# Performance work log

Measured on AMD Instinct MI355X. Metric: run time of the kernel, lower is better.

The kernel has to match this reference:

```python
import jax, jax.numpy as jnp
import numpy as np

N = 16384          # batch of signals
DIM_T = 256        # time steps per signal
DT = 0.01          # integration dt (intg_lev=1 -> dt_intg = dt)
NUF = 256          # num_units_feat
HID_XI = 128       # hidlayers_xi
HID_AUX = 64       # hidlayers_aux1_dec
LEN_INTG = DIM_T   # (dim_t-1)*intg_lev + 1 with intg_lev=1


def _linear_init(key, fan_in, fan_out):
    # torch nn.Linear default: U(-1/sqrt(fan_in), 1/sqrt(fan_in))
    s = 1.0 / np.sqrt(fan_in)
    kw, kb = jax.random.split(key)
    W = jax.random.uniform(kw, (fan_in, fan_out), minval=-s, maxval=s, dtype=jnp.float32)
    b = jax.random.uniform(kb, (fan_out,), minval=-s, maxval=s, dtype=jnp.float32)
    return W, b


def setup_inputs() -> dict:
    key = jax.random.key(0)
    ks = jax.random.split(key, 12)
    data = jax.random.normal(ks[0], (N, DIM_T), dtype=jnp.float32)
    omega = jax.random.normal(ks[1], (N, 1), dtype=jnp.float32)
    eps = jax.random.normal(ks[2], (N, 1), dtype=jnp.float32)
    # feature extractor (mlp branch): [dim_t+1 -> 256 -> 256], relu after both (actfun_output=True)
    W_feat1, b_feat1 = _linear_init(ks[3], DIM_T + 1, NUF)
    W_feat2, b_feat2 = _linear_init(ks[4], NUF, NUF)
    # xi mean head: MLP [256 -> 128 -> 1] then Softplus
    W_xim1, b_xim1 = _linear_init(ks[5], NUF, HID_XI)
    W_xim2, b_xim2 = _linear_init(ks[6], HID_XI, 1)
    # xi lnvar head: MLP [256 -> 128 -> 1]
    W_xil1, b_xil1 = _linear_init(ks[7], NUF, HID_XI)
    W_xil2, b_xil2 = _linear_init(ks[8], HID_XI, 1)
    # decoder aux1 MLP: [dim_z_aux1+1=2 -> 64 -> 1]
    W_aux1, b_aux1 = _linear_init(ks[9], 2, HID_AUX)
    W_aux2, b_aux2 = _linear_init(ks[10], HID_AUX, 1)
    return dict(data=data, omega=omega, eps=eps,
                W_feat1=W_feat1, b_feat1=b_feat1, W_feat2=W_feat2, b_feat2=b_feat2,
                W_xim1=W_xim1, b_xim1=b_xim1, W_xim2=W_xim2, b_xim2=b_xim2,
                W_xil1=W_xil1, b_xil1=b_xil1, W_xil2=W_xil2, b_xil2=b_xil2,
                W_aux1=W_aux1, b_aux1=b_aux1, W_aux2=W_aux2, b_aux2=b_aux2)


def reference(data, omega, eps,
              W_feat1, b_feat1, W_feat2, b_feat2,
              W_xim1, b_xim1, W_xim2, b_xim2,
              W_xil1, b_xil1, W_xil2, b_xil2,
              W_aux1, b_aux1, W_aux2, b_aux2):
    relu = jax.nn.relu
    # ---- encode_xi ----
    x_ = jnp.concatenate([data, omega], axis=1)                 # [n, dim_t+1]
    feat = relu(relu(x_ @ W_feat1 + b_feat1) @ W_feat2 + b_feat2)  # [n, 256]
    xi_mean = jax.nn.softplus(relu(feat @ W_xim1 + b_xim1) @ W_xim2 + b_xim2)  # [n, 1]
    xi_lnvar = relu(feat @ W_xil1 + b_xil1) @ W_xil2 + b_xil2                  # [n, 1]
    # ---- draw (reparameterization + clamp to feasible range [0, 1]) ----
    xi = xi_mean + jnp.exp(0.5 * xi_lnvar) * eps
    xi = jnp.clip(xi, 0.0, 1.0)
    # ---- decode: Euler odeint over LEN_INTG steps of state yy=[y, dy/dt] ----
    init_y = data[:, :1]                                        # [n, 1]
    initcond = jnp.concatenate([init_y, jnp.zeros_like(init_y)], axis=1)  # [n, 2]

    def step(yy, _):
        # physics: d[y, v]/dt = [v, 0]; aux MLP adds acceleration from (z_aux1=omega, y)
        aux_in = jnp.concatenate([omega, yy[:, :1]], axis=1)    # [n, 2]
        acc = relu(aux_in @ W_aux1 + b_aux1) @ W_aux2 + b_aux2  # [n, 1]
        dyy = jnp.concatenate([yy[:, 1:2], acc], axis=1)        # [n, 2]
        return yy + DT * dyy, yy

    _, yy_seq = jax.lax.scan(step, initcond, None, length=LEN_INTG)  # [len_intg, n, 2]
    y_seq = yy_seq[:, :, 0].T                                   # [n, dim_t] (intg_lev=1)
    t_intg = DT * jnp.arange(LEN_INTG, dtype=jnp.float32)       # [dim_t]
    x_PAB = jnp.exp(-jnp.abs(xi) * t_intg[None, :]) * y_seq     # [n, dim_t]
    return xi_mean, xi_lnvar, x_PAB
```

## Files before the change

kernel.cpp:

```cpp
#include <hip/hip_runtime.h>
#include <math.h>

#define NROWS 16384
#define DT_C 0.01f

typedef short s16x8 __attribute__((ext_vector_type(8)));
typedef float f32x4 __attribute__((ext_vector_type(4)));
typedef float f32x2 __attribute__((ext_vector_type(2)));

__device__ __forceinline__ unsigned short f2bf(float f) {
    unsigned u = __float_as_uint(f);
    u += 0x7fffu + ((u >> 16) & 1u);
    return (unsigned short)(u >> 16);
}
__device__ __forceinline__ unsigned pack2bf(float a, float b) {
    return (unsigned)f2bf(a) | ((unsigned)f2bf(b) << 16);
}
__device__ __forceinline__ float swz1(float v){ return __int_as_float(__builtin_amdgcn_ds_swizzle(__float_as_int(v), 0x041F)); }
__device__ __forceinline__ float swz2(float v){ return __int_as_float(__builtin_amdgcn_ds_swizzle(__float_as_int(v), 0x081F)); }
__device__ __forceinline__ float swz4(float v){ return __int_as_float(__builtin_amdgcn_ds_swizzle(__float_as_int(v), 0x101F)); }

__global__ __launch_bounds__(256) void prep_k(
    const float* __restrict__ Wf1, const float* __restrict__ Wf2,
    const float* __restrict__ Wm1, const float* __restrict__ Wl1,
    const float* __restrict__ bm1, const float* __restrict__ bl1,
    unsigned short* __restrict__ wpack, float* __restrict__ biasH)
{
    const int id = blockIdx.x * 256 + threadIdx.x;
    const int n  = id & 255;
    const int k8 = (id >> 8) & 31;
    const int s  = id >> 13;

    unsigned short tmp[8];
    #pragma unroll
    for (int j = 0; j < 8; ++j) {
        const int k = k8 * 8 + j;
        float v;
        if (s == 0)      v = Wf1[k * 256 + n];
        else if (s == 1) v = Wf2[k * 256 + n];
        else             v = (n < 128) ? Wm1[k * 128 + n] : Wl1[k * 128 + n - 128];
        tmp[j] = f2bf(v);
    }
    *(uint4*)&wpack[((s * 32 + k8) * 256 + n) * 8] = *(const uint4*)tmp;

    if (id < 256) biasH[id] = (id < 128) ? bm1[id] : bl1[id - 128];
}

__global__ __launch_bounds__(256, 2) void fused_k(
    const float* __restrict__ data, const float* __restrict__ omega,
    const float* __restrict__ eps_g,
    const unsigned short* __restrict__ wpack, const float* __restrict__ biasH,
    const float* __restrict__ bf1, const float* __restrict__ bf2,
    const float* __restrict__ w256g,
    const float* __restrict__ Wm2, const float* __restrict__ bm2,
    const float* __restrict__ Wl2, const float* __restrict__ bl2,
    const float* __restrict__ Wa1, const float* __restrict__ ba1,
    const float* __restrict__ Wa2, const float* __restrict__ ba2,
    float* __restrict__ out_mean, float* __restrict__ out_lnvar,
    float* __restrict__ xout)
{
    __shared__ unsigned short As1[8192];
    __shared__ unsigned short Hs[8192];
    __shared__ float headsF[32 * 256];
    __shared__ float omg[32];
    __shared__ float xiS[32];

    const int tid  = threadIdx.x;
    const int wid  = tid >> 6;
    const int lane = tid & 63;
    const int ln   = lane & 15;
    const int quad = lane >> 4;
    const int r0   = blockIdx.x * 32;

    {
        #pragma unroll
        for (int g2 = 0; g2 < 8; ++g2) {
            const int unit = g2 * 256 + tid;
            const int m    = unit >> 6;
            const int c16  = unit & 63;
            const int kblk = c16 >> 1;
            const int h    = c16 & 1;
            const float4 v = *(const float4*)&data[(size_t)(r0 + m) * 256 + c16 * 4];
            unsigned* d = (unsigned*)&As1[((kblk * 32) + (m ^ (kblk & 7))) * 8 + h * 4];
            d[0] = pack2bf(v.x, v.y);
            d[1] = pack2bf(v.z, v.w);
        }
        if (tid < 32) omg[tid] = omega[r0 + tid];
    }

    f32x4 acc[2][4];

    auto seed = [&](const float* bias) {
        #pragma unroll
        for (int nt = 0; nt < 4; ++nt) {
            const float b = bias[wid * 64 + nt * 16 + ln];
            acc[0][nt] = f32x4{b, b, b, b};
            acc[1][nt] = acc[0][nt];
        }
    };

    auto run_stage = [&](const unsigned short* Ap, const unsigned short* wp) {
        #pragma unroll
        for (int c = 0; c < 4; ++c) {
            #pragma unroll
            for (int kk = 0; kk < 2; ++kk) {
                const int kb   = kk * 4 + quad;
                const int kblk = c * 8 + kb;
                const int f    = kblk & 7;
                s16x8 b0 = *(const s16x8*)&wp[((size_t)(kblk * 256) + wid * 64 + 0 * 16 + ln) * 8];
                s16x8 b1 = *(const s16x8*)&wp[((size_t)(kblk * 256) + wid * 64 + 1 * 16 + ln) * 8];
                s16x8 b2 = *(const s16x8*)&wp[((size_t)(kblk * 256) + wid * 64 + 2 * 16 + ln) * 8];
                s16x8 b3 = *(const s16x8*)&wp[((size_t)(kblk * 256) + wid * 64 + 3 * 16 + ln) * 8];
                s16x8 a0 = *(const s16x8*)&Ap[(kblk * 32 + (ln ^ f)) * 8];
                s16x8 a1 = *(const s16x8*)&Ap[(kblk * 32 + ((ln ^ f) + 16)) * 8];
                acc[0][0] = __builtin_amdgcn_mfma_f32_16x16x32_bf16(a0, b0, acc[0][0], 0, 0, 0);
                acc[1][0] = __builtin_amdgcn_mfma_f32_16x16x32_bf16(a1, b0, acc[1][0], 0, 0, 0);
                acc[0][1] = __builtin_amdgcn_mfma_f32_16x16x32_bf16(a0, b1, acc[0][1], 0, 0, 0);
                acc[1][1] = __builtin_amdgcn_mfma_f32_16x16x32_bf16(a1, b1, acc[1][1], 0, 0, 0);
                acc[0][2] = __builtin_amdgcn_mfma_f32_16x16x32_bf16(a0, b2, acc[0][2], 0, 0, 0);
                acc[1][2] = __builtin_amdgcn_mfma_f32_16x16x32_bf16(a1, b2, acc[1][2], 0, 0, 0);
                acc[0][3] = __builtin_amdgcn_mfma_f32_16x16x32_bf16(a0, b3, acc[0][3], 0, 0, 0);
                acc[1][3] = __builtin_amdgcn_mfma_f32_16x16x32_bf16(a1, b3, acc[1][3], 0, 0, 0);
            }
        }
    };

    auto write_packed = [&](unsigned short* dst, bool addOm) {
        #pragma unroll
        for (int nt = 0; nt < 4; ++nt) {
            const int col = wid * 64 + nt * 16 + ln;
            const int kg  = col >> 3, f = kg & 7, jj = col & 7;
            const float wo = addOm ? w256g[col] : 0.f;
            #pragma unroll
            for (int mt = 0; mt < 2; ++mt) {
                #pragma unroll
                for (int r = 0; r < 4; ++r) {
                    const int row = mt * 16 + quad * 4 + r;
                    float v = acc[mt][nt][r];
                    if (addOm) v = fmaf(omg[row], wo, v);
                    v = fmaxf(v, 0.f);
                    dst[(kg * 32 + (row ^ f)) * 8 + jj] = f2bf(v);
                }
            }
        }
    };

    __syncthreads();
    seed(bf1);
    run_stage(As1, wpack);
    write_packed(Hs, true);
    __syncthreads();
    seed(bf2);
    run_stage(Hs, wpack + 65536);
    write_packed(As1, false);
    __syncthreads();
    seed(biasH);
    run_stage(As1, wpack + 131072);
    #pragma unroll
    for (int nt = 0; nt < 4; ++nt) {
        const int col = wid * 64 + nt * 16 + ln;
        #pragma unroll
        for (int mt = 0; mt < 2; ++mt) {
            #pragma unroll
            for (int r = 0; r < 4; ++r) {
                const int row = mt * 16 + quad * 4 + r;
                headsF[row * 256 + ((col + row * 8) & 255)] = fmaxf(acc[mt][nt][r], 0.f);
            }
        }
    }
    __syncthreads();

    {
        const int m = tid >> 3, l = tid & 7;
        float pm = 0.f, pl = 0.f;
        #pragma unroll
        for (int q = 0; q < 4; ++q) {
            const int c0 = l * 16 + q * 4;
            const float4 hm = *(const float4*)&headsF[m * 256 + ((c0 + m * 8) & 255)];
            const float4 wm = *(const float4*)&Wm2[c0];
            const float4 hl = *(const float4*)&headsF[m * 256 + ((128 + c0 + m * 8) & 255)];
            const float4 wl = *(const float4*)&Wl2[c0];
            pm = fmaf(hm.w, wm.w, fmaf(hm.z, wm.z, fmaf(hm.y, wm.y, fmaf(hm.x, wm.x, pm))));
            pl = fmaf(hl.w, wl.w, fmaf(hl.z, wl.z, fmaf(hl.y, wl.y, fmaf(hl.x, wl.x, pl))));
        }
        pm += swz1(pm); pm += swz2(pm); pm += swz4(pm);
        pl += swz1(pl); pl += swz2(pl); pl += swz4(pl);
        if (l == 0) {
            const float xm  = pm + bm2[0];
            const float mean = fmaxf(xm, 0.f) + log1pf(expf(-fabsf(xm)));
            const float lnv  = pl + bl2[0];
            out_mean[r0 + m]  = mean;
            out_lnvar[r0 + m] = lnv;
            float xi = mean + expf(0.5f * lnv) * eps_g[r0 + m];
            xiS[m] = fminf(fmaxf(xi, 0.f), 1.f);
        }
    }
    __syncthreads();

    {
        const int r   = tid >> 3;
        const int l   = tid & 7;
        const int row = r0 + r;
        const float om = omg[r];
        const float xi = xiS[r];
        const float s  = expf(-xi * DT_C);
        const float pseed = ba2[0] * 0.125f;

        f32x2 w1v[4], Av[4], w2v[4];
        #pragma unroll
        for (int i = 0; i < 4; ++i) {
            const f32x2 w0 = *(const f32x2*)&Wa1[l * 8 + i * 2];
            const f32x2 bb = *(const f32x2*)&ba1[l * 8 + i * 2];
            w1v[i] = *(const f32x2*)&Wa1[64 + l * 8 + i * 2];
            w2v[i] = *(const f32x2*)&Wa2[l * 8 + i * 2];
            Av[i]  = f32x2{fmaf(om, w0.x, bb.x), fmaf(om, w0.y, bb.y)};
        }

        auto partial = [&](float y) -> float {
            const f32x2 y2 = f32x2{y, y};
            f32x2 acc2 = f32x2{pseed, 0.f};
            #pragma unroll
            for (int i = 0; i < 4; ++i) {
                f32x2 h = __builtin_elementwise_fma(y2, w1v[i], Av[i]);
                h = __builtin_elementwise_max(h, f32x2{0.f, 0.f});
                acc2 = __builtin_elementwise_fma(h, w2v[i], acc2);
            }
            return acc2.x + acc2.y;
        };

        const float y0 = data[(size_t)row * 256];
        float ym = y0;
        float yc = y0;
        const float DT2 = DT_C * DT_C;

        float p = partial(ym);
        p += swz1(p); p += swz2(p); p += swz4(p);
        float pr = p;

        float d = 1.f;
        float* orow = xout + (size_t)row * 256 + l * 4;

        for (int tb = 0; tb < 8; ++tb) {
            float cur[4];
            #pragma unroll
            for (int j = 0; j < 32; ++j) {
                const float m_ = d * ym;
                if ((j >> 2) == l) cur[j & 3] = m_;
                d *= s;
                float pn = partial(yc);
                pn += swz1(pn); pn += swz2(pn); pn += swz4(pn);
                const float ynext = fmaf(DT2, pr, fmaf(2.f, yc, -ym));
                ym = yc; yc = ynext; pr = pn;
            }
            *(float4*)&orow[tb * 32] = *(const float4*)cur;
        }
    }
}

extern "C" void kernel_launch(void* const* d_in, const int* in_sizes, int n_in,
                              void* d_out, int out_size, void* d_ws, size_t ws_size,
                              hipStream_t stream)
{
    const float* data    = (const float*)d_in[0];
    const float* omega   = (const float*)d_in[1];
    const float* eps     = (const float*)d_in[2];
    const float* W_feat1 = (const float*)d_in[3];
    const float* b_feat1 = (const float*)d_in[4];
    const float* W_feat2 = (const float*)d_in[5];
    const float* b_feat2 = (const float*)d_in[6];
    const float* W_xim1  = (const float*)d_in[7];
    const float* b_xim1  = (const float*)d_in[8];
    const float* W_xim2  = (const float*)d_in[9];
    const float* b_xim2  = (const float*)d_in[10];
    const float* W_xil1  = (const float*)d_in[11];
    const float* b_xil1  = (const float*)d_in[12];
    const float* W_xil2  = (const float*)d_in[13];
    const float* b_xil2  = (const float*)d_in[14];
    const float* W_aux1  = (const float*)d_in[15];
    const float* b_aux1  = (const float*)d_in[16];
    const float* W_aux2  = (const float*)d_in[17];
    const float* b_aux2  = (const float*)d_in[18];

    float* out_mean  = (float*)d_out;
    float* out_lnvar = out_mean + NROWS;
    float* out_x     = out_lnvar + NROWS;

    unsigned short* wpack = (unsigned short*)d_ws;
    float* biasH = (float*)((char*)d_ws + 3 * 32 * 256 * 8 * 2);

    prep_k<<<96, 256, 0, stream>>>(W_feat1, W_feat2, W_xim1, W_xil1,
                                   b_xim1, b_xil1, wpack, biasH);
    fused_k<<<512, 256, 0, stream>>>(data, omega, eps, wpack, biasH,
                                     b_feat1, b_feat2, W_feat1 + 256 * 256,
                                     W_xim2, b_xim2, W_xil2, b_xil2,
                                     W_aux1, b_aux1, W_aux2, b_aux2,
                                     out_mean, out_lnvar, out_x);
}
```

Before: 145.7 us.

## Run ODE integration before MLP encoder and apply decay as a post-pass

The Euler recurrence for y no longer depends on xi, so it now runs first, right after the data tile is loaded, and writes the raw y trajectory to the output. The exp(-xi·t) decay is applied afterwards by reading back and rescaling the output row. Cross-lane reductions switch from ds_swizzle to DPP row operations, and shared memory is aliased (headsF overlays the A/H buffers) with an extra barrier so occupancy can rise. The cost is an extra global read and write of the full output plus the use of __expf, which is less precise than the old running product.

```diff
diff --git a/kernel.cpp b/kernel.cpp
--- a/kernel.cpp
+++ b/kernel.cpp
@@ -16,9 +16,17 @@
 __device__ __forceinline__ unsigned pack2bf(float a, float b) {
     return (unsigned)f2bf(a) | ((unsigned)f2bf(b) << 16);
 }
-__device__ __forceinline__ float swz1(float v){ return __int_as_float(__builtin_amdgcn_ds_swizzle(__float_as_int(v), 0x041F)); }
-__device__ __forceinline__ float swz2(float v){ return __int_as_float(__builtin_amdgcn_ds_swizzle(__float_as_int(v), 0x081F)); }
-__device__ __forceinline__ float swz4(float v){ return __int_as_float(__builtin_amdgcn_ds_swizzle(__float_as_int(v), 0x101F)); }
+template <int CTRL>
+__device__ __forceinline__ float dppadd(float v) {
+    int x = __builtin_amdgcn_update_dpp(0, __float_as_int(v), CTRL, 0xF, 0xF, true);
+    return v + __int_as_float(x);
+}
+__device__ __forceinline__ float sum8(float p) {
+    p = dppadd<0xB1>(p);
+    p = dppadd<0x4E>(p);
+    p = dppadd<0x141>(p);
+    return p;
+}
 
 __global__ __launch_bounds__(256) void prep_k(
     const float* __restrict__ Wf1, const float* __restrict__ Wf2,
@@ -59,11 +67,12 @@
     float* __restrict__ out_mean, float* __restrict__ out_lnvar,
     float* __restrict__ xout)
 {
-    __shared__ unsigned short As1[8192];
-    __shared__ unsigned short Hs[8192];
-    __shared__ float headsF[32 * 256];
-    __shared__ float omg[32];
-    __shared__ float xiS[32];
+    __shared__ __align__(16) unsigned char smem[33024];
+    unsigned short* As1 = (unsigned short*)smem;
+    unsigned short* Hs  = (unsigned short*)(smem + 16384);
+    float* headsF = (float*)smem;
+    float* omg = (float*)(smem + 32768);
+    float* xiS = omg + 32;
 
     const int tid  = threadIdx.x;
     const int wid  = tid >> 6;
@@ -86,6 +95,56 @@
             d[1] = pack2bf(v.z, v.w);
         }
         if (tid < 32) omg[tid] = omega[r0 + tid];
+    }
+    __syncthreads();
+
+    {
+        const int r   = tid >> 3;
+        const int l   = tid & 7;
+        const int row = r0 + r;
+        const float om = omg[r];
+        const float pseed = ba2[0] * 0.125f;
+
+        f32x2 w1v[4], Av[4], w2v[4];
+        #pragma unroll
+        for (int i = 0; i < 4; ++i) {
+            const f32x2 w0 = *(const f32x2*)&Wa1[l * 8 + i * 2];
+            const f32x2 bb = *(const f32x2*)&ba1[l * 8 + i * 2];
+            w1v[i] = *(const f32x2*)&Wa1[64 + l * 8 + i * 2];
+            w2v[i] = *(const f32x2*)&Wa2[l * 8 + i * 2];
+            Av[i]  = f32x2{fmaf(om, w0.x, bb.x), fmaf(om, w0.y, bb.y)};
+        }
+
+        auto partial = [&](float y) -> float {
+            const f32x2 y2 = f32x2{y, y};
+            f32x2 acc2 = f32x2{pseed, 0.f};
+            #pragma unroll
+            for (int i = 0; i < 4; ++i) {
+                f32x2 h = __builtin_elementwise_fma(y2, w1v[i], Av[i]);
+                h = __builtin_elementwise_max(h, f32x2{0.f, 0.f});
+                acc2 = __builtin_elementwise_fma(h, w2v[i], acc2);
+            }
+            return acc2.x + acc2.y;
+        };
+
+        const float y0 = data[(size_t)row * 256];
+        float ym = y0;
+        float yc = y0;
+        const float DT2 = DT_C * DT_C;
+        float pr = sum8(partial(ym));
+
+        float* orow = xout + (size_t)row * 256 + l * 4;
+        for (int tb = 0; tb < 8; ++tb) {
+            float cur[4];
+            #pragma unroll
+            for (int j = 0; j < 32; ++j) {
+                if ((j >> 2) == l) cur[j & 3] = ym;
+                float pn = sum8(partial(yc));
+                const float ynext = fmaf(DT2, pr, fmaf(2.f, yc, -ym));
+                ym = yc; yc = ynext; pr = pn;
+            }
+            *(float4*)&orow[tb * 32] = *(const float4*)cur;
+        }
     }
 
     f32x4 acc[2][4];
@@ -145,7 +204,6 @@
         }
     };
 
-    __syncthreads();
     seed(bf1);
     run_stage(As1, wpack);
     write_packed(Hs, true);
@@ -156,6 +214,7 @@
     __syncthreads();
     seed(biasH);
     run_stage(As1, wpack + 131072);
+    __syncthreads();
     #pragma unroll
     for (int nt = 0; nt < 4; ++nt) {
         const int col = wid * 64 + nt * 16 + ln;
@@ -183,8 +242,8 @@
             pm = fmaf(hm.w, wm.w, fmaf(hm.z, wm.z, fmaf(hm.y, wm.y, fmaf(hm.x, wm.x, pm))));
             pl = fmaf(hl.w, wl.w, fmaf(hl.z, wl.z, fmaf(hl.y, wl.y, fmaf(hl.x, wl.x, pl))));
         }
-        pm += swz1(pm); pm += swz2(pm); pm += swz4(pm);
-        pl += swz1(pl); pl += swz2(pl); pl += swz4(pl);
+        pm = sum8(pm);
+        pl = sum8(pl);
         if (l == 0) {
             const float xm  = pm + bm2[0];
             const float mean = fmaxf(xm, 0.f) + log1pf(expf(-fabsf(xm)));
@@ -200,59 +259,17 @@
     {
         const int r   = tid >> 3;
         const int l   = tid & 7;
-        const int row = r0 + r;
-        const float om = omg[r];
-        const float xi = xiS[r];
-        const float s  = expf(-xi * DT_C);
-        const float pseed = ba2[0] * 0.125f;
-
-        f32x2 w1v[4], Av[4], w2v[4];
-        #pragma unroll
-        for (int i = 0; i < 4; ++i) {
-            const f32x2 w0 = *(const f32x2*)&Wa1[l * 8 + i * 2];
-            const f32x2 bb = *(const f32x2*)&ba1[l * 8 + i * 2];
-            w1v[i] = *(const f32x2*)&Wa1[64 + l * 8 + i * 2];
-            w2v[i] = *(const f32x2*)&Wa2[l * 8 + i * 2];
-            Av[i]  = f32x2{fmaf(om, w0.x, bb.x), fmaf(om, w0.y, bb.y)};
-        }
-
-        auto partial = [&](float y) -> float {
-            const f32x2 y2 = f32x2{y, y};
-            f32x2 acc2 = f32x2{pseed, 0.f};
-            #pragma unroll
-            for (int i = 0; i < 4; ++i) {
-                f32x2 h = __builtin_elementwise_fma(y2, w1v[i], Av[i]);
-                h = __builtin_elementwise_max(h, f32x2{0.f, 0.f});
-                acc2 = __builtin_elementwise_fma(h, w2v[i], acc2);
-            }
-            return acc2.x + acc2.y;
-        };
-
-        const float y0 = data[(size_t)row * 256];
-        float ym = y0;
-        float yc = y0;
-        const float DT2 = DT_C * DT_C;
-
-        float p = partial(ym);
-        p += swz1(p); p += swz2(p); p += swz4(p);
-        float pr = p;
-
-        float d = 1.f;
-        float* orow = xout + (size_t)row * 256 + l * 4;
-
+        const float nxdt = -xiS[r] * DT_C;
+        float* orow = xout + (size_t)(r0 + r) * 256 + l * 4;
+        #pragma unroll
         for (int tb = 0; tb < 8; ++tb) {
-            float cur[4];
-            #pragma unroll
-            for (int j = 0; j < 32; ++j) {
-                const float m_ = d * ym;
-                if ((j >> 2) == l) cur[j & 3] = m_;
-                d *= s;
-                float pn = partial(yc);
-                pn += swz1(pn); pn += swz2(pn); pn += swz4(pn);
-                const float ynext = fmaf(DT2, pr, fmaf(2.f, yc, -ym));
-                ym = yc; yc = ynext; pr = pn;
-            }
-            *(float4*)&orow[tb * 32] = *(const float4*)cur;
+            float4 v = *(const float4*)&orow[tb * 32];
+            const int c0 = tb * 32 + l * 4;
+            v.x *= __expf(nxdt * (float)(c0 + 0));
+            v.y *= __expf(nxdt * (float)(c0 + 1));
+            v.z *= __expf(nxdt * (float)(c0 + 2));
+            v.w *= __expf(nxdt * (float)(c0 + 3));
+            *(float4*)&orow[tb * 32] = v;
         }
     }
 }
```

Measured after the change: 139.9 us. -4.0%, faster.
